# Performance work log

Measured on AMD Instinct MI355X. Metric: run time of the kernel, lower is better.

The kernel has to match this reference:

```python
import jax, jax.numpy as jnp
import numpy as np

N = 100_000      # nodes
E = 1_600_000    # edges (avg degree 16)
IN_DIM = 128
HID = 512
NCLS = 64
BN_EPS = 1e-5


def setup_inputs() -> dict:
    key = jax.random.key(0)
    ks = jax.random.split(key, 16)

    def lin(k, fi, fo):
        kw, kb = jax.random.split(k)
        s = 1.0 / np.sqrt(fi)
        return (jax.random.uniform(kw, (fi, fo), jnp.float32, -s, s),
                jax.random.uniform(kb, (fo,), jnp.float32, -s, s))

    W1a, b1a = lin(ks[2], IN_DIM, HID)
    W1b, b1b = lin(ks[3], HID, HID)
    W2a, b2a = lin(ks[4], HID, HID)
    W2b, b2b = lin(ks[5], HID, NCLS)
    return {
        "x": jax.random.normal(ks[0], (N, IN_DIM), jnp.float32),
        "edge_index": jax.random.randint(ks[1], (2, E), 0, N, jnp.int32),
        "g": jnp.zeros((1,), jnp.int32),
        "A_k": jnp.zeros((1,), jnp.int32),
        "D": jnp.zeros((1,), jnp.int32),
        "Kindices": jnp.zeros((1,), jnp.int32),
        "de": jnp.zeros((1,), jnp.int32),
        "M": jnp.zeros((1,), jnp.int32),
        "I": jnp.zeros((1,), jnp.int32),
        "W1a": W1a, "b1a": b1a, "W1b": W1b, "b1b": b1b,
        "gamma1": jnp.ones((HID,), jnp.float32), "beta1": jnp.zeros((HID,), jnp.float32),
        "W2a": W2a, "b2a": b2a, "W2b": W2b, "b2b": b2b,
        "gamma2": jnp.ones((NCLS,), jnp.float32), "beta2": jnp.zeros((NCLS,), jnp.float32),
    }


def _gin_conv(x, src, dst, Wa, ba, Wb, bb):
    # PyG GINConv (eps=0): nn(x + sum_{j in N(i)} x_j); messages x[src] summed at dst
    agg = jax.ops.segment_sum(x[src], dst, num_segments=N)
    h = x + agg
    h = jax.nn.relu(h @ Wa + ba)
    return h @ Wb + bb


def _batchnorm(x, gamma, beta):
    # training-mode BatchNorm1d: batch stats over node dim, biased variance
    mu = jnp.mean(x, axis=0)
    var = jnp.mean(jnp.square(x - mu), axis=0)
    return gamma * (x - mu) * jax.lax.rsqrt(var + BN_EPS) + beta


def reference(x, edge_index, g, A_k, D, Kindices, de, M, I,
              W1a, b1a, W1b, b1b, gamma1, beta1,
              W2a, b2a, W2b, b2b, gamma2, beta2):
    src, dst = edge_index[0], edge_index[1]
    h = jax.nn.selu(_gin_conv(x, src, dst, W1a, b1a, W1b, b1b))
    h = _batchnorm(h, gamma1, beta1)
    # dropout(p=0.5) omitted (eval-mode / deterministic reference)
    h = jax.nn.selu(_gin_conv(h, src, dst, W2a, b2a, W2b, b2b))
    h = _batchnorm(h, gamma2, beta2)
    return jax.nn.softmax(h, axis=1)
```

## Files before the change

kernel.cpp:

```cpp
#include <hip/hip_runtime.h>
#include <hip/hip_bf16.h>

#define N_NODES 100000
#define N_EDGES 1600000
#define IN_DIM 128
#define HID 512
#define NCLS 64

typedef __attribute__((ext_vector_type(8))) short bf16x8;
typedef __attribute__((ext_vector_type(4))) float f32x4;

__device__ inline float bf2f(unsigned short b) {
    unsigned int u = ((unsigned int)b) << 16;
    return __builtin_bit_cast(float, u);
}
__device__ inline unsigned short f2bf(float f) {
    unsigned int u = __builtin_bit_cast(unsigned int, f);
    unsigned int lsb = (u >> 16) & 1u;
    u += 0x7fffu + lsb;
    return (unsigned short)(u >> 16);
}
__device__ inline float selu_f(float x) {
    const float scale = 1.0507009873554805f;
    const float alpha = 1.6732632423543772f;
    return x > 0.f ? scale * x : scale * alpha * (__expf(x) - 1.f);
}
__device__ inline void stb(float* p, float v) { *p = v; }
__device__ inline void stb(unsigned short* p, float v) { *p = f2bf(v); }

__device__ inline void gl_lds16(const void* g, void* l) {
    __builtin_amdgcn_global_load_lds((const __attribute__((address_space(1))) void*)g,
                                     (__attribute__((address_space(3))) void*)l, 16, 0, 0);
}

__global__ __launch_bounds__(256) void k_cast(const float* __restrict__ x,
                                              unsigned short* __restrict__ xb) {
    size_t g = (size_t)blockIdx.x * 256 + threadIdx.x;
    size_t total = (size_t)N_NODES * IN_DIM / 8;
    if (g >= total) return;
    const float4* p = (const float4*)(x + g * 8);
    float4 v0 = p[0], v1 = p[1];
    uint4 o;
    o.x = (unsigned)f2bf(v0.x) | ((unsigned)f2bf(v0.y) << 16);
    o.y = (unsigned)f2bf(v0.z) | ((unsigned)f2bf(v0.w) << 16);
    o.z = (unsigned)f2bf(v1.x) | ((unsigned)f2bf(v1.y) << 16);
    o.w = (unsigned)f2bf(v1.z) | ((unsigned)f2bf(v1.w) << 16);
    ((uint4*)xb)[g] = o;
}

__global__ __launch_bounds__(256) void k_deg(const int* __restrict__ dst, int* __restrict__ deg) {
    int e = blockIdx.x * 256 + threadIdx.x;
    if (e < N_EDGES) atomicAdd(&deg[dst[e]], 1);
}

#define SCAN_NB 98

__global__ __launch_bounds__(256) void k_scan_part(const int* __restrict__ deg, int* __restrict__ part) {
    __shared__ int sd[256];
    int b = blockIdx.x, t = threadIdx.x;
    int i0 = b * 1024 + t * 4;
    int s = 0;
#pragma unroll
    for (int k = 0; k < 4; ++k) if (i0 + k < N_NODES) s += deg[i0 + k];
    sd[t] = s;
    __syncthreads();
    for (int o = 128; o > 0; o >>= 1) {
        if (t < o) sd[t] += sd[t + o];
        __syncthreads();
    }
    if (t == 0) part[b] = sd[0];
}

__global__ __launch_bounds__(128) void k_scan_mid(const int* __restrict__ part, int* __restrict__ base,
                                                  int* __restrict__ off) {
    __shared__ int sp[128];
    int t = threadIdx.x;
    int v = (t < SCAN_NB) ? part[t] : 0;
    sp[t] = v;
    __syncthreads();
    for (int o = 1; o < 128; o <<= 1) {
        int tv = (t >= o) ? sp[t - o] : 0;
        __syncthreads();
        sp[t] += tv;
        __syncthreads();
    }
    if (t < SCAN_NB) base[t] = sp[t] - v;
    if (t == SCAN_NB - 1) off[N_NODES] = sp[t];
}

__global__ __launch_bounds__(256) void k_scan_fin(const int* __restrict__ deg, const int* __restrict__ base,
                                                  int* __restrict__ off, int* __restrict__ pos) {
    __shared__ int sd[256];
    int b = blockIdx.x, t = threadIdx.x;
    int i0 = b * 1024 + t * 4;
    int v[4]; int s = 0;
#pragma unroll
    for (int k = 0; k < 4; ++k) { v[k] = (i0 + k < N_NODES) ? deg[i0 + k] : 0; s += v[k]; }
    sd[t] = s;
    __syncthreads();
    for (int o = 1; o < 256; o <<= 1) {
        int tv = (t >= o) ? sd[t - o] : 0;
        __syncthreads();
        sd[t] += tv;
        __syncthreads();
    }
    int excl = base[b] + sd[t] - s;
#pragma unroll
    for (int k = 0; k < 4; ++k) {
        if (i0 + k < N_NODES) { off[i0 + k] = excl; pos[i0 + k] = excl; excl += v[k]; }
    }
}

__global__ __launch_bounds__(256) void k_fill(const int* __restrict__ src, const int* __restrict__ dst,
                                              int* __restrict__ pos, int* __restrict__ adj) {
    int e = blockIdx.x * 256 + threadIdx.x;
    if (e < N_EDGES) {
        int p = atomicAdd(&pos[dst[e]], 1);
        adj[p] = src[e];
    }
}

__global__ __launch_bounds__(256) void k_pack(const float* __restrict__ W,
                                              unsigned short* __restrict__ Wp, int K, int NC) {
    int idx = blockIdx.x * 256 + threadIdx.x;
    if (idx >= K * NC) return;
    int j = idx & 7;
    int l = (idx >> 3) & 63;
    int t = idx >> 9;
    int KT = K >> 5;
    int kt = t % KT;
    int nt = t / KT;
    int k = kt * 32 + (l >> 4) * 8 + j;
    int n = nt * 16 + (l & 15);
    Wp[idx] = f2bf(W[(size_t)k * NC + n]);
}

__global__ __launch_bounds__(256) void k_packT(const float* __restrict__ W,
                                               unsigned short* __restrict__ WT, int K, int NC) {
    int idx = blockIdx.x * 256 + threadIdx.x;
    if (idx >= K * NC) return;
    int k = idx & (K - 1);
    int n = idx / K;
    WT[idx] = f2bf(W[(size_t)k * NC + n]);
}

__global__ __launch_bounds__(256) void k_agg1(const unsigned short* __restrict__ xb,
                                              const int* __restrict__ off, const int* __restrict__ adj,
                                              unsigned short* __restrict__ A1) {
    int w = (blockIdx.x * 256 + threadIdx.x) >> 6;
    if (w >= N_NODES) return;
    int lane = threadIdx.x & 63;
    unsigned v = ((const unsigned*)(xb + (size_t)w * IN_DIM))[lane];
    float s0 = bf2f((unsigned short)(v & 0xffff));
    float s1 = bf2f((unsigned short)(v >> 16));
    int e0 = off[w], e1 = off[w + 1];
    int e = e0;
    for (; e + 4 <= e1; e += 4) {
        int j0 = adj[e], j1 = adj[e + 1], j2 = adj[e + 2], j3 = adj[e + 3];
        unsigned u0 = ((const unsigned*)(xb + (size_t)j0 * IN_DIM))[lane];
        unsigned u1 = ((const unsigned*)(xb + (size_t)j1 * IN_DIM))[lane];
        unsigned u2 = ((const unsigned*)(xb + (size_t)j2 * IN_DIM))[lane];
        unsigned u3 = ((const unsigned*)(xb + (size_t)j3 * IN_DIM))[lane];
        s0 += bf2f((unsigned short)(u0 & 0xffff)) + bf2f((unsigned short)(u1 & 0xffff)) +
              bf2f((unsigned short)(u2 & 0xffff)) + bf2f((unsigned short)(u3 & 0xffff));
        s1 += bf2f((unsigned short)(u0 >> 16)) + bf2f((unsigned short)(u1 >> 16)) +
              bf2f((unsigned short)(u2 >> 16)) + bf2f((unsigned short)(u3 >> 16));
    }
    for (; e < e1; ++e) {
        unsigned u = ((const unsigned*)(xb + (size_t)adj[e] * IN_DIM))[lane];
        s0 += bf2f((unsigned short)(u & 0xffff));
        s1 += bf2f((unsigned short)(u >> 16));
    }
    ((unsigned*)(A1 + (size_t)w * IN_DIM))[lane] = (unsigned)f2bf(s0) | ((unsigned)f2bf(s1) << 16);
}

__global__ __launch_bounds__(256) void k_aggbn2(const unsigned short* __restrict__ h,
                                                const int* __restrict__ off, const int* __restrict__ adj,
                                                const float* __restrict__ bn,
                                                unsigned short* __restrict__ outb) {
    int w = (blockIdx.x * 256 + threadIdx.x) >> 6;
    if (w >= N_NODES) return;
    int lane = threadIdx.x & 63;
    int fb = blockIdx.y * 256 + lane * 4;
    const unsigned short* hp = h + fb;
    float scl[4], shf[4];
#pragma unroll
    for (int k = 0; k < 4; ++k) {
        scl[k] = bn[2 * HID + fb + k];
        shf[k] = bn[3 * HID + fb + k];
    }
    uint2 v = *(const uint2*)(hp + (size_t)w * HID);
    float s0 = bf2f((unsigned short)(v.x & 0xffff));
    float s1 = bf2f((unsigned short)(v.x >> 16));
    float s2 = bf2f((unsigned short)(v.y & 0xffff));
    float s3 = bf2f((unsigned short)(v.y >> 16));
    int e0 = off[w], e1 = off[w + 1];
    int e = e0;
    for (; e + 4 <= e1; e += 4) {
        int j0 = adj[e], j1 = adj[e + 1], j2 = adj[e + 2], j3 = adj[e + 3];
        uint2 u0 = *(const uint2*)(hp + (size_t)j0 * HID);
        uint2 u1 = *(const uint2*)(hp + (size_t)j1 * HID);
        uint2 u2 = *(const uint2*)(hp + (size_t)j2 * HID);
        uint2 u3 = *(const uint2*)(hp + (size_t)j3 * HID);
        s0 += bf2f((unsigned short)(u0.x & 0xffff)) + bf2f((unsigned short)(u1.x & 0xffff)) +
              bf2f((unsigned short)(u2.x & 0xffff)) + bf2f((unsigned short)(u3.x & 0xffff));
        s1 += bf2f((unsigned short)(u0.x >> 16)) + bf2f((unsigned short)(u1.x >> 16)) +
              bf2f((unsigned short)(u2.x >> 16)) + bf2f((unsigned short)(u3.x >> 16));
        s2 += bf2f((unsigned short)(u0.y & 0xffff)) + bf2f((unsigned short)(u1.y & 0xffff)) +
              bf2f((unsigned short)(u2.y & 0xffff)) + bf2f((unsigned short)(u3.y & 0xffff));
        s3 += bf2f((unsigned short)(u0.y >> 16)) + bf2f((unsigned short)(u1.y >> 16)) +
              bf2f((unsigned short)(u2.y >> 16)) + bf2f((unsigned short)(u3.y >> 16));
    }
    for (; e < e1; ++e) {
        uint2 u = *(const uint2*)(hp + (size_t)adj[e] * HID);
        s0 += bf2f((unsigned short)(u.x & 0xffff));
        s1 += bf2f((unsigned short)(u.x >> 16));
        s2 += bf2f((unsigned short)(u.y & 0xffff));
        s3 += bf2f((unsigned short)(u.y >> 16));
    }
    float dp1 = (float)(e1 - e0 + 1);
    float r0 = s0 * scl[0] + dp1 * shf[0];
    float r1 = s1 * scl[1] + dp1 * shf[1];
    float r2 = s2 * scl[2] + dp1 * shf[2];
    float r3 = s3 * scl[3] + dp1 * shf[3];
    unsigned long long o =
        (unsigned long long)((unsigned)f2bf(r0) | ((unsigned)f2bf(r1) << 16)) |
        ((unsigned long long)((unsigned)f2bf(r2) | ((unsigned)f2bf(r3) << 16)) << 32);
    __builtin_nontemporal_store(o, (unsigned long long*)(outb + (size_t)w * HID + fb));
}

template <int K, int ACT>
__global__ __launch_bounds__(256) void k_tgemm(const unsigned short* __restrict__ A,
                                               const unsigned short* __restrict__ WT,
                                               const float* __restrict__ bias,
                                               unsigned short* __restrict__ Out, int M) {
    constexpr int NC = 512;
    __shared__ __align__(16) char smem[32768];
    const int tid = threadIdx.x;
    const int lane = tid & 63;
    const int w = tid >> 6;
    const int wm = w >> 1, wn = w & 1;
    const int l15 = lane & 15, lg = lane >> 4;
    const int rowbase = blockIdx.y * 128;
    const int colbase = blockIdx.x * 128;

    f32x4 acc[4][4];
#pragma unroll
    for (int i = 0; i < 4; ++i)
#pragma unroll
        for (int j = 0; j < 4; ++j) acc[i][j] = (f32x4)0.f;

    for (int k0 = 0; k0 < K; k0 += 64) {
#pragma unroll
        for (int i = 0; i < 4; ++i) {
            int slot = i * 256 + tid;
            int r = slot >> 3;
            int u = (slot & 7) ^ (r & 7);
            int gr = rowbase + r; if (gr >= M) gr = M - 1;
            gl_lds16(A + (size_t)gr * K + k0 + u * 8, smem + (i * 256 + w * 64) * 16);
        }
#pragma unroll
        for (int i = 0; i < 4; ++i) {
            int slot = i * 256 + tid;
            int c = slot >> 3;
            int u = (slot & 7) ^ (c & 7);
            gl_lds16(WT + (size_t)(colbase + c) * K + k0 + u * 8,
                     smem + 16384 + (i * 256 + w * 64) * 16);
        }
        __syncthreads();
#pragma unroll
        for (int kin = 0; kin < 2; ++kin) {
            bf16x8 af[4], bfr[4];
#pragma unroll
            for (int mi = 0; mi < 4; ++mi) {
                int r = wm * 64 + mi * 16 + l15;
                int u = (kin * 4 + lg) ^ (r & 7);
                af[mi] = *(const bf16x8*)(smem + r * 128 + u * 16);
            }
#pragma unroll
            for (int ni = 0; ni < 4; ++ni) {
                int c = wn * 64 + ni * 16 + l15;
                int u = (kin * 4 + lg) ^ (c & 7);
                bfr[ni] = *(const bf16x8*)(smem + 16384 + c * 128 + u * 16);
            }
#pragma unroll
            for (int mi = 0; mi < 4; ++mi)
#pragma unroll
                for (int ni = 0; ni < 4; ++ni)
                    acc[mi][ni] = __builtin_amdgcn_mfma_f32_16x16x32_bf16(af[mi], bfr[ni], acc[mi][ni], 0, 0, 0);
        }
        __syncthreads();
    }

#pragma unroll
    for (int ni = 0; ni < 4; ++ni) {
        int c = wn * 64 + ni * 16 + l15;
        float bv = bias[colbase + c];
#pragma unroll
        for (int mi = 0; mi < 4; ++mi) {
#pragma unroll
            for (int r = 0; r < 4; ++r) {
                int row = wm * 64 + mi * 16 + lg * 4 + r;
                float t = acc[mi][ni][r] + bv;
                t = (ACT == 0) ? fmaxf(t, 0.f) : selu_f(t);
                int byte = (row * 256 + c * 2) ^ ((row & 7) << 4);
                *(unsigned short*)(smem + byte) = f2bf(t);
            }
        }
    }
    __syncthreads();
#pragma unroll
    for (int it = 0; it < 8; ++it) {
        int idx = it * 256 + tid;
        int row = idx >> 4;
        int ch = idx & 15;
        int gr = rowbase + row;
        if (gr < M) {
            uint4 v = *(const uint4*)(smem + row * 256 + ((ch ^ (row & 7)) << 4));
            *(uint4*)(Out + (size_t)gr * NC + colbase + ch * 8) = v;
        }
    }
}

template <int K, int NC, int ACT, int WAVES_M, int WAVES_N, int NFRAG, typename TOUT>
__global__ __launch_bounds__(WAVES_M * WAVES_N * 64) void k_mgemm(
    const unsigned short* __restrict__ A, const unsigned short* __restrict__ Wp,
    const float* __restrict__ bias, TOUT* __restrict__ Out, int M) {
    const int tid = threadIdx.x;
    const int lane = tid & 63;
    const int w = tid >> 6;
    const int wm = w / WAVES_N;
    const int wn = w % WAVES_N;
    const int l15 = lane & 15;
    const int lg = lane >> 4;
    const int rowbase = blockIdx.x * (32 * WAVES_M) + wm * 32;
    const int colbase = blockIdx.y * (WAVES_N * 16 * NFRAG) + wn * 16 * NFRAG;
    int r0 = rowbase + l15; if (r0 > M - 1) r0 = M - 1;
    int r1 = rowbase + 16 + l15; if (r1 > M - 1) r1 = M - 1;
    const unsigned short* pa0 = A + (size_t)r0 * K + lg * 8;
    const unsigned short* pa1 = A + (size_t)r1 * K + lg * 8;
    const unsigned short* pw = Wp + (size_t)(colbase >> 4) * (K / 32) * 512 + lane * 8;

    f32x4 acc[2][NFRAG];
#pragma unroll
    for (int i = 0; i < 2; ++i)
#pragma unroll
        for (int j = 0; j < NFRAG; ++j) acc[i][j] = (f32x4)0.f;

#pragma unroll 2
    for (int kt = 0; kt < K / 32; ++kt) {
        bf16x8 a0 = *(const bf16x8*)(pa0 + kt * 32);
        bf16x8 a1 = *(const bf16x8*)(pa1 + kt * 32);
#pragma unroll
        for (int ni = 0; ni < NFRAG; ++ni) {
            bf16x8 bv = *(const bf16x8*)(pw + (ni * (K / 32) + kt) * 512);
            acc[0][ni] = __builtin_amdgcn_mfma_f32_16x16x32_bf16(a0, bv, acc[0][ni], 0, 0, 0);
            acc[1][ni] = __builtin_amdgcn_mfma_f32_16x16x32_bf16(a1, bv, acc[1][ni], 0, 0, 0);
        }
    }

#pragma unroll
    for (int ni = 0; ni < NFRAG; ++ni) {
        int c = colbase + ni * 16 + l15;
        float bv = bias[c];
#pragma unroll
        for (int mi = 0; mi < 2; ++mi) {
#pragma unroll
            for (int r = 0; r < 4; ++r) {
                int row = rowbase + mi * 16 + lg * 4 + r;
                if (row < M) {
                    float t = acc[mi][ni][r] + bv;
                    t = (ACT == 0) ? fmaxf(t, 0.f) : selu_f(t);
                    stb(&Out[(size_t)row * NC + c], t);
                }
            }
        }
    }
}

__global__ __launch_bounds__(256) void k_bnstats_h(const unsigned short* __restrict__ C,
                                                   float* __restrict__ sums) {
    int t = threadIdx.x;
    float s0 = 0, q0 = 0, s1 = 0, q1 = 0;
    for (int r = blockIdx.x; r < N_NODES; r += gridDim.x) {
        unsigned v = ((const unsigned*)(C + (size_t)r * HID))[t];
        float a = bf2f((unsigned short)(v & 0xffff));
        float b = bf2f((unsigned short)(v >> 16));
        s0 += a; q0 += a * a;
        s1 += b; q1 += b * b;
    }
    atomicAdd(&sums[2 * t], s0);
    atomicAdd(&sums[2 * t + 1], s1);
    atomicAdd(&sums[HID + 2 * t], q0);
    atomicAdd(&sums[HID + 2 * t + 1], q1);
}

__global__ void k_bnprep(float* __restrict__ bn, const float* __restrict__ gamma,
                         const float* __restrict__ beta, int C, float invn) {
    int c = threadIdx.x + blockIdx.x * blockDim.x;
    if (c >= C) return;
    float mu = bn[c] * invn;
    float var = bn[C + c] * invn - mu * mu;
    float sc = gamma[c] * rsqrtf(var + 1e-5f);
    bn[2 * C + c] = sc;
    bn[3 * C + c] = beta[c] - mu * sc;
}

__global__ __launch_bounds__(256) void k_bnstats_o(const float* __restrict__ O,
                                                   float* __restrict__ bn2) {
    int t = threadIdx.x;
    int c = t & 63;
    int rr = t >> 6;
    float s = 0, q = 0;
    for (int r = blockIdx.x * 4 + rr; r < N_NODES; r += gridDim.x * 4) {
        float a = O[(size_t)r * NCLS + c];
        s += a; q += a * a;
    }
    atomicAdd(&bn2[c], s);
    atomicAdd(&bn2[NCLS + c], q);
}

__global__ __launch_bounds__(256) void k_softmax(float* __restrict__ O, const float* __restrict__ bn2) {
    int w = (blockIdx.x * 256 + threadIdx.x) >> 6;
    if (w >= N_NODES) return;
    int lane = threadIdx.x & 63;
    float z = O[(size_t)w * NCLS + lane] * bn2[2 * NCLS + lane] + bn2[3 * NCLS + lane];
    float m = z;
#pragma unroll
    for (int o = 32; o > 0; o >>= 1) m = fmaxf(m, __shfl_xor(m, o));
    float e = __expf(z - m);
    float s = e;
#pragma unroll
    for (int o = 32; o > 0; o >>= 1) s += __shfl_xor(s, o);
    O[(size_t)w * NCLS + lane] = e / s;
}

extern "C" void kernel_launch(void* const* d_in, const int* in_sizes, int n_in,
                              void* d_out, int out_size, void* d_ws, size_t ws_size,
                              hipStream_t stream) {
    const float* x = (const float*)d_in[0];
    const int* edge = (const int*)d_in[1];
    const int* srcp = edge;
    const int* dstp = edge + N_EDGES;
    const float* W1a = (const float*)d_in[9];
    const float* b1a = (const float*)d_in[10];
    const float* W1b = (const float*)d_in[11];
    const float* b1b = (const float*)d_in[12];
    const float* gamma1 = (const float*)d_in[13];
    const float* beta1 = (const float*)d_in[14];
    const float* W2a = (const float*)d_in[15];
    const float* b2a = (const float*)d_in[16];
    const float* W2b = (const float*)d_in[17];
    const float* b2b = (const float*)d_in[18];
    const float* gamma2 = (const float*)d_in[19];
    const float* beta2 = (const float*)d_in[20];
    float* out = (float*)d_out;

    char* ws = (char*)d_ws;
    size_t o = 0;
    auto alloc = [&](size_t bytes) -> char* {
        char* p = ws + o;
        o = (o + bytes + 255) & ~(size_t)255;
        return p;
    };
    int* off = (int*)alloc((N_NODES + 1) * sizeof(int));
    int* deg = (int*)alloc(N_NODES * sizeof(int));
    int* pos = (int*)alloc(N_NODES * sizeof(int));
    int* adj = (int*)alloc(N_EDGES * sizeof(int));
    int* part = (int*)alloc(SCAN_NB * sizeof(int));
    int* base = (int*)alloc(SCAN_NB * sizeof(int));
    float* bn1 = (float*)alloc(4 * HID * sizeof(float));
    float* bn2 = (float*)alloc(4 * NCLS * sizeof(float));
    unsigned short* WT1 = (unsigned short*)alloc((size_t)IN_DIM * HID * sizeof(unsigned short));
    unsigned short* WT2 = (unsigned short*)alloc((size_t)HID * HID * sizeof(unsigned short));
    unsigned short* WT3 = (unsigned short*)alloc((size_t)HID * HID * sizeof(unsigned short));
    unsigned short* Wp4 = (unsigned short*)alloc((size_t)HID * NCLS * sizeof(unsigned short));
    unsigned short* xb = (unsigned short*)alloc((size_t)N_NODES * IN_DIM * sizeof(unsigned short));
    unsigned short* A1 = (unsigned short*)alloc((size_t)N_NODES * IN_DIM * sizeof(unsigned short));
    unsigned short* B = (unsigned short*)alloc((size_t)N_NODES * HID * sizeof(unsigned short));
    unsigned short* C = (unsigned short*)alloc((size_t)N_NODES * HID * sizeof(unsigned short));

    hipMemsetAsync(deg, 0, N_NODES * sizeof(int), stream);
    hipMemsetAsync(bn1, 0, 2 * HID * sizeof(float), stream);
    hipMemsetAsync(bn2, 0, 2 * NCLS * sizeof(float), stream);

    int eb = (N_EDGES + 255) / 256;
    k_cast<<<(N_NODES * IN_DIM / 8 + 255) / 256, 256, 0, stream>>>(x, xb);
    k_deg<<<eb, 256, 0, stream>>>(dstp, deg);
    k_scan_part<<<SCAN_NB, 256, 0, stream>>>(deg, part);
    k_scan_mid<<<1, 128, 0, stream>>>(part, base, off);
    k_scan_fin<<<SCAN_NB, 256, 0, stream>>>(deg, base, off, pos);
    k_fill<<<eb, 256, 0, stream>>>(srcp, dstp, pos, adj);

    k_packT<<<(IN_DIM * HID) / 256, 256, 0, stream>>>(W1a, WT1, IN_DIM, HID);
    k_packT<<<(HID * HID) / 256, 256, 0, stream>>>(W1b, WT2, HID, HID);
    k_packT<<<(HID * HID) / 256, 256, 0, stream>>>(W2a, WT3, HID, HID);
    k_pack<<<(HID * NCLS) / 256, 256, 0, stream>>>(W2b, Wp4, HID, NCLS);

    int nwb = (N_NODES * 64 + 255) / 256;
    int mb128 = (N_NODES + 127) / 128;

    k_agg1<<<nwb, 256, 0, stream>>>(xb, off, adj, A1);
    k_tgemm<IN_DIM, 0><<<dim3(4, mb128), 256, 0, stream>>>(A1, WT1, b1a, B, N_NODES);
    k_tgemm<HID, 1><<<dim3(4, mb128), 256, 0, stream>>>(B, WT2, b1b, C, N_NODES);

    k_bnstats_h<<<1024, 256, 0, stream>>>(C, bn1);
    k_bnprep<<<2, 256, 0, stream>>>(bn1, gamma1, beta1, HID, 1.0f / N_NODES);

    k_aggbn2<<<dim3(nwb, 2), 256, 0, stream>>>(C, off, adj, bn1, B);

    k_tgemm<HID, 0><<<dim3(4, mb128), 256, 0, stream>>>(B, WT3, b2a, C, N_NODES);
    k_mgemm<HID, NCLS, 1, 8, 1, 4, float><<<dim3((N_NODES + 255) / 256, 1), 512, 0, stream>>>(C, Wp4, b2b, out, N_NODES);

    k_bnstats_o<<<1024, 256, 0, stream>>>(out, bn2);
    k_bnprep<<<1, 64, 0, stream>>>(bn2, gamma2, beta2, NCLS, 1.0f / N_NODES);
    k_softmax<<<nwb, 256, 0, stream>>>(out, bn2);
}
```

Baseline: 1.018 ms.

## Fuse BN1 statistics into GEMM epilogue, remap GEMM grid, split agg1 edges

The second layer-1 GEMM now accumulates per-column sum and sum-of-squares in its epilogue and writes per-block partials. A small reduction kernel turns these into BN scale and shift, which removes the separate pass over the 100k×512 activation and its atomics. The GEMM grid becomes 1D with blocks grouped so that eight row tiles and all four column tiles run close together, aiming for better L2 reuse of A. agg1 now has each half-wave handle alternate edges with 8-byte loads, then combines the halves with a shuffle. Risks are a one-pass variance that can lose precision, and a serial 782-step loop in the reduction kernel.

```diff
diff --git a/kernel.cpp b/kernel.cpp
--- a/kernel.cpp
+++ b/kernel.cpp
@@ -9,6 +9,10 @@
 
 typedef __attribute__((ext_vector_type(8))) short bf16x8;
 typedef __attribute__((ext_vector_type(4))) float f32x4;
+
+#define RB_COUNT 782
+#define RB_PAD 784
+#define TG_GRID (RB_PAD * 4)
 
 __device__ inline float bf2f(unsigned short b) {
     unsigned int u = ((unsigned int)b) << 16;
@@ -150,28 +154,52 @@
     int w = (blockIdx.x * 256 + threadIdx.x) >> 6;
     if (w >= N_NODES) return;
     int lane = threadIdx.x & 63;
-    unsigned v = ((const unsigned*)(xb + (size_t)w * IN_DIM))[lane];
-    float s0 = bf2f((unsigned short)(v & 0xffff));
-    float s1 = bf2f((unsigned short)(v >> 16));
+    int f4 = (lane & 31) * 4;
+    int eo = lane >> 5;
+    const unsigned short* base = xb + f4;
+    float s0 = 0.f, s1 = 0.f, s2 = 0.f, s3 = 0.f;
+    if (eo == 0) {
+        uint2 v = *(const uint2*)(base + (size_t)w * IN_DIM);
+        s0 = bf2f((unsigned short)(v.x & 0xffff));
+        s1 = bf2f((unsigned short)(v.x >> 16));
+        s2 = bf2f((unsigned short)(v.y & 0xffff));
+        s3 = bf2f((unsigned short)(v.y >> 16));
+    }
     int e0 = off[w], e1 = off[w + 1];
-    int e = e0;
-    for (; e + 4 <= e1; e += 4) {
-        int j0 = adj[e], j1 = adj[e + 1], j2 = adj[e + 2], j3 = adj[e + 3];
-        unsigned u0 = ((const unsigned*)(xb + (size_t)j0 * IN_DIM))[lane];
-        unsigned u1 = ((const unsigned*)(xb + (size_t)j1 * IN_DIM))[lane];
-        unsigned u2 = ((const unsigned*)(xb + (size_t)j2 * IN_DIM))[lane];
-        unsigned u3 = ((const unsigned*)(xb + (size_t)j3 * IN_DIM))[lane];
-        s0 += bf2f((unsigned short)(u0 & 0xffff)) + bf2f((unsigned short)(u1 & 0xffff)) +
-              bf2f((unsigned short)(u2 & 0xffff)) + bf2f((unsigned short)(u3 & 0xffff));
-        s1 += bf2f((unsigned short)(u0 >> 16)) + bf2f((unsigned short)(u1 >> 16)) +
-              bf2f((unsigned short)(u2 >> 16)) + bf2f((unsigned short)(u3 >> 16));
-    }
-    for (; e < e1; ++e) {
-        unsigned u = ((const unsigned*)(xb + (size_t)adj[e] * IN_DIM))[lane];
-        s0 += bf2f((unsigned short)(u & 0xffff));
-        s1 += bf2f((unsigned short)(u >> 16));
-    }
-    ((unsigned*)(A1 + (size_t)w * IN_DIM))[lane] = (unsigned)f2bf(s0) | ((unsigned)f2bf(s1) << 16);
+    int pb = e0;
+    for (; pb + 8 <= e1; pb += 8) {
+        int i0 = adj[pb + eo], i1 = adj[pb + 2 + eo], i2 = adj[pb + 4 + eo], i3 = adj[pb + 6 + eo];
+        uint2 u0 = *(const uint2*)(base + (size_t)i0 * IN_DIM);
+        uint2 u1 = *(const uint2*)(base + (size_t)i1 * IN_DIM);
+        uint2 u2 = *(const uint2*)(base + (size_t)i2 * IN_DIM);
+        uint2 u3 = *(const uint2*)(base + (size_t)i3 * IN_DIM);
+        s0 += bf2f((unsigned short)(u0.x & 0xffff)) + bf2f((unsigned short)(u1.x & 0xffff)) +
+              bf2f((unsigned short)(u2.x & 0xffff)) + bf2f((unsigned short)(u3.x & 0xffff));
+        s1 += bf2f((unsigned short)(u0.x >> 16)) + bf2f((unsigned short)(u1.x >> 16)) +
+              bf2f((unsigned short)(u2.x >> 16)) + bf2f((unsigned short)(u3.x >> 16));
+        s2 += bf2f((unsigned short)(u0.y & 0xffff)) + bf2f((unsigned short)(u1.y & 0xffff)) +
+              bf2f((unsigned short)(u2.y & 0xffff)) + bf2f((unsigned short)(u3.y & 0xffff));
+        s3 += bf2f((unsigned short)(u0.y >> 16)) + bf2f((unsigned short)(u1.y >> 16)) +
+              bf2f((unsigned short)(u2.y >> 16)) + bf2f((unsigned short)(u3.y >> 16));
+    }
+    for (int idx = pb + eo; idx < e1; idx += 2) {
+        int j = adj[idx];
+        uint2 u = *(const uint2*)(base + (size_t)j * IN_DIM);
+        s0 += bf2f((unsigned short)(u.x & 0xffff));
+        s1 += bf2f((unsigned short)(u.x >> 16));
+        s2 += bf2f((unsigned short)(u.y & 0xffff));
+        s3 += bf2f((unsigned short)(u.y >> 16));
+    }
+    s0 += __shfl_xor(s0, 32);
+    s1 += __shfl_xor(s1, 32);
+    s2 += __shfl_xor(s2, 32);
+    s3 += __shfl_xor(s3, 32);
+    if (eo == 0) {
+        uint2 o;
+        o.x = (unsigned)f2bf(s0) | ((unsigned)f2bf(s1) << 16);
+        o.y = (unsigned)f2bf(s2) | ((unsigned)f2bf(s3) << 16);
+        *(uint2*)(A1 + (size_t)w * IN_DIM + f4) = o;
+    }
 }
 
 __global__ __launch_bounds__(256) void k_aggbn2(const unsigned short* __restrict__ h,
@@ -229,20 +257,28 @@
     __builtin_nontemporal_store(o, (unsigned long long*)(outb + (size_t)w * HID + fb));
 }
 
-template <int K, int ACT>
+template <int K, int ACT, int STATS>
 __global__ __launch_bounds__(256) void k_tgemm(const unsigned short* __restrict__ A,
                                                const unsigned short* __restrict__ WT,
                                                const float* __restrict__ bias,
-                                               unsigned short* __restrict__ Out, int M) {
+                                               unsigned short* __restrict__ Out,
+                                               float* __restrict__ scratch, int M) {
     constexpr int NC = 512;
-    __shared__ __align__(16) char smem[32768];
+    __shared__ __align__(16) char smem[32768 + 2048];
+    const int bid = blockIdx.x;
+    const int r8 = bid & 7;
+    const int q = bid >> 3;
+    const int cb = q & 3;
+    const int rb = (q >> 2) * 8 + r8;
+    const int rowbase = rb * 128;
+    const int colbase = cb * 128;
+    if (rowbase >= M) return;
+
     const int tid = threadIdx.x;
     const int lane = tid & 63;
     const int w = tid >> 6;
     const int wm = w >> 1, wn = w & 1;
     const int l15 = lane & 15, lg = lane >> 4;
-    const int rowbase = blockIdx.y * 128;
-    const int colbase = blockIdx.x * 128;
 
     f32x4 acc[4][4];
 #pragma unroll
@@ -292,6 +328,11 @@
         __syncthreads();
     }
 
+    float cs[4], cq[4];
+    if (STATS) {
+#pragma unroll
+        for (int ni = 0; ni < 4; ++ni) { cs[ni] = 0.f; cq[ni] = 0.f; }
+    }
 #pragma unroll
     for (int ni = 0; ni < 4; ++ni) {
         int c = wn * 64 + ni * 16 + l15;
@@ -303,8 +344,23 @@
                 int row = wm * 64 + mi * 16 + lg * 4 + r;
                 float t = acc[mi][ni][r] + bv;
                 t = (ACT == 0) ? fmaxf(t, 0.f) : selu_f(t);
+                if (STATS && (rowbase + row < M)) { cs[ni] += t; cq[ni] += t * t; }
                 int byte = (row * 256 + c * 2) ^ ((row & 7) << 4);
                 *(unsigned short*)(smem + byte) = f2bf(t);
+            }
+        }
+    }
+    if (STATS) {
+        float* sS = (float*)(smem + 32768);
+#pragma unroll
+        for (int ni = 0; ni < 4; ++ni) {
+            float a = cs[ni];
+            a += __shfl_xor(a, 16); a += __shfl_xor(a, 32);
+            float b = cq[ni];
+            b += __shfl_xor(b, 16); b += __shfl_xor(b, 32);
+            if (lg == 0) {
+                sS[wm * 256 + (wn * 64 + ni * 16 + l15)] = a;
+                sS[wm * 256 + 128 + (wn * 64 + ni * 16 + l15)] = b;
             }
         }
     }
@@ -320,6 +376,32 @@
             *(uint4*)(Out + (size_t)gr * NC + colbase + ch * 8) = v;
         }
     }
+    if (STATS) {
+        const float* sS = (const float*)(smem + 32768);
+        int c = tid & 127, kind = tid >> 7;
+        float v = sS[kind * 128 + c] + sS[256 + kind * 128 + c];
+        scratch[(size_t)(rb * 4 + cb) * 256 + kind * 128 + c] = v;
+    }
+}
+
+__global__ __launch_bounds__(64) void k_bnred(const float* __restrict__ scratch,
+                                              const float* __restrict__ gamma,
+                                              const float* __restrict__ beta,
+                                              float* __restrict__ bn) {
+    int c = blockIdx.x * 64 + threadIdx.x;
+    int cbk = c >> 7, cl = c & 127;
+    float s = 0.f, qq = 0.f;
+    for (int rb = 0; rb < RB_COUNT; ++rb) {
+        const float* p = scratch + (size_t)(rb * 4 + cbk) * 256;
+        s += p[cl];
+        qq += p[128 + cl];
+    }
+    float invn = 1.0f / N_NODES;
+    float mu = s * invn;
+    float var = qq * invn - mu * mu;
+    float sc = gamma[c] * rsqrtf(var + 1e-5f);
+    bn[2 * HID + c] = sc;
+    bn[3 * HID + c] = beta[c] - mu * sc;
 }
 
 template <int K, int NC, int ACT, int WAVES_M, int WAVES_N, int NFRAG, typename TOUT>
@@ -378,21 +460,18 @@
     }
 }
 
-__global__ __launch_bounds__(256) void k_bnstats_h(const unsigned short* __restrict__ C,
-                                                   float* __restrict__ sums) {
+__global__ __launch_bounds__(256) void k_bnstats_o(const float* __restrict__ O,
+                                                   float* __restrict__ bn2) {
     int t = threadIdx.x;
-    float s0 = 0, q0 = 0, s1 = 0, q1 = 0;
-    for (int r = blockIdx.x; r < N_NODES; r += gridDim.x) {
-        unsigned v = ((const unsigned*)(C + (size_t)r * HID))[t];
-        float a = bf2f((unsigned short)(v & 0xffff));
-        float b = bf2f((unsigned short)(v >> 16));
-        s0 += a; q0 += a * a;
-        s1 += b; q1 += b * b;
-    }
-    atomicAdd(&sums[2 * t], s0);
-    atomicAdd(&sums[2 * t + 1], s1);
-    atomicAdd(&sums[HID + 2 * t], q0);
-    atomicAdd(&sums[HID + 2 * t + 1], q1);
+    int c = t & 63;
+    int rr = t >> 6;
+    float s = 0, q = 0;
+    for (int r = blockIdx.x * 4 + rr; r < N_NODES; r += gridDim.x * 4) {
+        float a = O[(size_t)r * NCLS + c];
+        s += a; q += a * a;
+    }
+    atomicAdd(&bn2[c], s);
+    atomicAdd(&bn2[NCLS + c], q);
 }
 
 __global__ void k_bnprep(float* __restrict__ bn, const float* __restrict__ gamma,
@@ -404,20 +483,6 @@
     float sc = gamma[c] * rsqrtf(var + 1e-5f);
     bn[2 * C + c] = sc;
     bn[3 * C + c] = beta[c] - mu * sc;
-}
-
-__global__ __launch_bounds__(256) void k_bnstats_o(const float* __restrict__ O,
-                                                   float* __restrict__ bn2) {
-    int t = threadIdx.x;
-    int c = t & 63;
-    int rr = t >> 6;
-    float s = 0, q = 0;
-    for (int r = blockIdx.x * 4 + rr; r < N_NODES; r += gridDim.x * 4) {
-        float a = O[(size_t)r * NCLS + c];
-        s += a; q += a * a;
-    }
-    atomicAdd(&bn2[c], s);
-    atomicAdd(&bn2[NCLS + c], q);
 }
 
 __global__ __launch_bounds__(256) void k_softmax(float* __restrict__ O, const float* __restrict__ bn2) {
@@ -471,6 +536,7 @@
     int* base = (int*)alloc(SCAN_NB * sizeof(int));
     float* bn1 = (float*)alloc(4 * HID * sizeof(float));
     float* bn2 = (float*)alloc(4 * NCLS * sizeof(float));
+    float* stat = (float*)alloc((size_t)RB_COUNT * 4 * 256 * sizeof(float));
     unsigned short* WT1 = (unsigned short*)alloc((size_t)IN_DIM * HID * sizeof(unsigned short));
     unsigned short* WT2 = (unsigned short*)alloc((size_t)HID * HID * sizeof(unsigned short));
     unsigned short* WT3 = (unsigned short*)alloc((size_t)HID * HID * sizeof(unsigned short));
@@ -481,7 +547,6 @@
     unsigned short* C = (unsigned short*)alloc((size_t)N_NODES * HID * sizeof(unsigned short));
 
     hipMemsetAsync(deg, 0, N_NODES * sizeof(int), stream);
-    hipMemsetAsync(bn1, 0, 2 * HID * sizeof(float), stream);
     hipMemsetAsync(bn2, 0, 2 * NCLS * sizeof(float), stream);
 
     int eb = (N_EDGES + 255) / 256;
@@ -498,18 +563,14 @@
     k_pack<<<(HID * NCLS) / 256, 256, 0, stream>>>(W2b, Wp4, HID, NCLS);
 
     int nwb = (N_NODES * 64 + 255) / 256;
-    int mb128 = (N_NODES + 127) / 128;
 
     k_agg1<<<nwb, 256, 0, stream>>>(xb, off, adj, A1);
-    k_tgemm<IN_DIM, 0><<<dim3(4, mb128), 256, 0, stream>>>(A1, WT1, b1a, B, N_NODES);
-    k_tgemm<HID, 1><<<dim3(4, mb128), 256, 0, stream>>>(B, WT2, b1b, C, N_NODES);
-
-    k_bnstats_h<<<1024, 256, 0, stream>>>(C, bn1);
-    k_bnprep<<<2, 256, 0, stream>>>(bn1, gamma1, beta1, HID, 1.0f / N_NODES);
+    k_tgemm<IN_DIM, 0, 0><<<TG_GRID, 256, 0, stream>>>(A1, WT1, b1a, B, nullptr, N_NODES);
+    k_tgemm<HID, 1, 1><<<TG_GRID, 256, 0, stream>>>(B, WT2, b1b, C, stat, N_NODES);
+    k_bnred<<<8, 64, 0, stream>>>(stat, gamma1, beta1, bn1);
 
     k_aggbn2<<<dim3(nwb, 2), 256, 0, stream>>>(C, off, adj, bn1, B);
-
-    k_tgemm<HID, 0><<<dim3(4, mb128), 256, 0, stream>>>(B, WT3, b2a, C, N_NODES);
+    k_tgemm<HID, 0, 0><<<TG_GRID, 256, 0, stream>>>(B, WT3, b2a, C, nullptr, N_NODES);
     k_mgemm<HID, NCLS, 1, 8, 1, 4, float><<<dim3((N_NODES + 255) / 256, 1), 512, 0, stream>>>(C, Wp4, b2b, out, N_NODES);
 
     k_bnstats_o<<<1024, 256, 0, stream>>>(out, bn2);
```

New measurement: 1.034 ms. No clear change (+1.6%).
